# Optimization experiments

Hardware: AMD Instinct MI355X
Metric: run time of the kernel (lower is better)

Reference implementation:

```python
import jax, jax.numpy as jnp
import numpy as np
from jax import lax

DIM = 256
NI, NS, NP = 8, 4, 16
H = W = 36
SCALE = 20.0
POOL = 4
EPS_BN = 1e-5


def setup_inputs() -> dict:
    key = jax.random.key(0)
    ks = jax.random.split(key, 20)
    feat = jax.random.normal(ks[0], (NI, NS, DIM, H, W), jnp.float32)
    # proposals in xywh; scaled by 20 inside PrRoIPool, so keep boxes inside the 36x36 map
    xy = jax.random.uniform(ks[1], (NI, NS, NP, 2), jnp.float32) * 1.2
    wh = 0.1 + jax.random.uniform(ks[2], (NI, NS, NP, 2), jnp.float32) * 0.4
    proposals = jnp.concatenate([xy, wh], axis=-1)

    def kaiming(k, shape, fan_in):
        return jax.random.normal(k, shape, jnp.float32) * np.float32(np.sqrt(2.0 / fan_in))

    d = dict(feat=feat, proposals=proposals)
    for i, name in enumerate(['conv1', 'conv2', 'conv3']):
        d[name + '_w'] = kaiming(ks[3 + i], (DIM, DIM, 3, 3), DIM * 9)
        d[name + '_b'] = jnp.zeros((DIM,), jnp.float32)
        d['bn%d_g' % (i + 1)] = jax.random.uniform(ks[6 + i], (DIM,), jnp.float32)
        d['bn%d_b' % (i + 1)] = jnp.zeros((DIM,), jnp.float32)
    d['fc_w'] = kaiming(ks[9], (DIM, DIM * POOL * POOL), DIM * POOL * POOL)
    d['fc_b'] = jnp.zeros((DIM,), jnp.float32)
    d['fcbn_g'] = jax.random.uniform(ks[10], (DIM,), jnp.float32)
    d['fcbn_b'] = jnp.zeros((DIM,), jnp.float32)
    d['iou_w'] = kaiming(ks[11], (1, DIM), DIM)
    d['iou_b'] = jnp.zeros((1,), jnp.float32)
    return d


def _cbr(x, w, b, g, beta):
    # Conv(3x3, pad 1) + BatchNorm (training-mode batch stats) + ReLU
    x = lax.conv_general_dilated(x, w, (1, 1), ((1, 1), (1, 1)),
                                 dimension_numbers=('NCHW', 'OIHW', 'NCHW'))
    x = x + b[None, :, None, None]
    m = x.mean((0, 2, 3), keepdims=True)
    v = x.var((0, 2, 3), keepdims=True)
    x = (x - m) / jnp.sqrt(v + EPS_BN) * g[None, :, None, None] + beta[None, :, None, None]
    return jax.nn.relu(x)


def _trapcum_last(a):
    # trapezoidal cumulative integral along last axis, value 0 at index 0
    mid = 0.5 * (a[..., :-1] + a[..., 1:])
    return jnp.concatenate([jnp.zeros_like(a[..., :1]), jnp.cumsum(mid, axis=-1)], axis=-1)


def _prroi_pool(feat, rois, pooled=POOL, scale=SCALE):
    # Precise RoI pooling: exact double integral of the bilinear interpolant per bin,
    # computed analytically via trapezoidal cumulative integrals of the feature map.
    N, C, Hh, Ww = feat.shape
    Ux = _trapcum_last(feat)                                            # int_0^x f
    Uy = jnp.swapaxes(_trapcum_last(jnp.swapaxes(feat, -1, -2)), -1, -2)  # int_0^y f
    T = jnp.swapaxes(_trapcum_last(jnp.swapaxes(Ux, -1, -2)), -1, -2)     # int_0^y int_0^x f

    b = rois[:, 0].astype(jnp.int32)
    x1, y1, x2, y2 = (rois[:, 1] * scale, rois[:, 2] * scale,
                      rois[:, 3] * scale, rois[:, 4] * scale)
    bw = (x2 - x1) / pooled
    bh = (y2 - y1) / pooled
    grid = jnp.arange(pooled + 1, dtype=feat.dtype)
    xs = jnp.clip(x1[:, None] + bw[:, None] * grid, 0.0, Ww - 1)        # (R, P+1)
    ys = jnp.clip(y1[:, None] + bh[:, None] * grid, 0.0, Hh - 1)
    wx = jnp.clip(jnp.floor(xs), 0, Ww - 2).astype(jnp.int32)
    hy = jnp.clip(jnp.floor(ys), 0, Hh - 2).astype(jnp.int32)
    sx = xs - wx.astype(feat.dtype)
    sy = ys - hy.astype(feat.dtype)
    px1 = 0.5 * sx * sx
    px0 = sx - px1
    py1 = 0.5 * sy * sy
    py0 = sy - py1

    def g(arr, hi, wi):
        # gather per-RoI values -> (R, P+1, P+1, C), rows index y, cols index x
        return arr[b[:, None, None], :, hi[:, :, None], wi[:, None, :]]

    px0e = px0[:, None, :, None]
    px1e = px1[:, None, :, None]
    py0e = py0[:, :, None, None]
    py1e = py1[:, :, None, None]
    h0, h1 = hy, hy + 1
    w0, w1 = wx, wx + 1
    # antiderivative G(X, Y) = int_0^Y int_0^X f of the bilinear interpolant
    G = (g(T, h0, w0)
         + g(Uy, h0, w0) * px0e + g(Uy, h0, w1) * px1e
         + py0e * (g(Ux, h0, w0) + g(feat, h0, w0) * px0e + g(feat, h0, w1) * px1e)
         + py1e * (g(Ux, h1, w0) + g(feat, h1, w0) * px0e + g(feat, h1, w1) * px1e))
    # per-bin integral via inclusion-exclusion on the (P+1)x(P+1) corner grid
    d = G[:, 1:, 1:] - G[:, :-1, 1:] - G[:, 1:, :-1] + G[:, :-1, :-1]   # (R, P, P, C)
    area = (bw * bh)[:, None, None, None]
    out = jnp.where(area > 1e-8, d / jnp.maximum(area, 1e-8), 0.0)
    return jnp.transpose(out, (0, 3, 1, 2))  # (R, C, P, P)


def reference(feat, proposals, conv1_w, conv1_b, bn1_g, bn1_b, conv2_w, conv2_b,
              bn2_g, bn2_b, conv3_w, conv3_b, bn3_g, bn3_b, fc_w, fc_b,
              fcbn_g, fcbn_b, iou_w, iou_b):
    ni, ns = proposals.shape[0], proposals.shape[1]
    x = feat.reshape(-1, *feat.shape[-3:])
    x = _cbr(x, conv1_w, conv1_b, bn1_g, bn1_b)
    x = _cbr(x, conv2_w, conv2_b, bn2_g, bn2_b)
    x = _cbr(x, conv3_w, conv3_b, bn3_g, bn3_b)

    props = proposals.reshape(ni * ns, -1, 4)
    B, P = props.shape[0], props.shape[1]
    xyxy = jnp.concatenate([props[..., 0:2], props[..., 0:2] + props[..., 2:4]], axis=-1)
    bidx = jnp.broadcast_to(jnp.arange(B, dtype=props.dtype)[:, None, None], (B, P, 1))
    rois = jnp.concatenate([bidx, xyxy], axis=-1).reshape(-1, 5)

    rf = _prroi_pool(x, rois)                       # (B*P, C, 4, 4)
    fcx = rf.reshape(rf.shape[0], -1) @ fc_w.T + fc_b
    m = fcx.mean(0)
    v = fcx.var(0)
    fcx = jax.nn.relu((fcx - m) / jnp.sqrt(v + EPS_BN) * fcbn_g + fcbn_b)
    iou = fcx @ iou_w.T + iou_b                     # (B*P, 1)
    return iou.reshape(ni, ns, -1)
```

## Files before the change

kernel.cpp:

```cpp
#include <hip/hip_runtime.h>
#include <hip/hip_bf16.h>
#include <stdint.h>

#define CDIM 256
#define HH 36
#define WW 36
#define NPX 1296
#define PW 38
#define PPIX 1444
#define NIMG 32
#define NROI 512
#define FCK 4096
#define EPS_BN 1e-5f
#define SBLK 192

typedef __bf16 bf16;
typedef __bf16 bf16x8 __attribute__((ext_vector_type(8)));
typedef float f32x4 __attribute__((ext_vector_type(4)));
typedef unsigned short us8 __attribute__((ext_vector_type(8)));

#define GLD16(g, l) __builtin_amdgcn_global_load_lds( \
    (__attribute__((address_space(1))) void*)(g),     \
    (__attribute__((address_space(3))) void*)(l), 16, 0, 0)

__global__ void k_wconv3(const float* __restrict__ w0, const float* __restrict__ w1,
                         const float* __restrict__ w2, bf16* __restrict__ wb) {
  int l = blockIdx.y;
  const float* ws = (l == 0) ? w0 : (l == 1) ? w1 : w2;
  bf16* dst = wb + (size_t)l * 9 * CDIM * CDIM;
  int i = blockIdx.x * 256 + threadIdx.x;
  if (i >= 9 * CDIM * CDIM) return;
  int tap = i / (CDIM * CDIM);
  int rem = i - tap * (CDIM * CDIM);
  int co = rem >> 8, ci = rem & 255;
  dst[i] = (bf16)ws[(size_t)(co * CDIM + ci) * 9 + tap];
}

__global__ void k_cast(const float* __restrict__ src, bf16* __restrict__ dst, int nElem) {
  int i = blockIdx.x * 256 + threadIdx.x;
  if (i < nElem) dst[i] = (bf16)src[i];
}

__global__ void k_convert(const float* __restrict__ feat, bf16* __restrict__ xp) {
  __shared__ bf16 tile[CDIM * 38];
  int h = blockIdx.x, n = blockIdx.y, t = threadIdx.x;
  const float* src = feat + (size_t)n * CDIM * NPX + (size_t)h * WW;
#pragma unroll 4
  for (int i = 0; i < 36; ++i) {
    int f = i * 256 + t;
    int c = (int)(((unsigned)f * 7282u) >> 18);
    int w = f - c * 36;
    tile[c * 38 + w] = (bf16)src[(size_t)c * NPX + w];
  }
  __syncthreads();
  bf16* dst = xp + (size_t)n * PPIX * CDIM + ((h + 1) * PW + 1) * CDIM + t;
#pragma unroll 4
  for (int w = 0; w < 36; ++w) dst[w * CDIM] = tile[t * 38 + w];
}

__global__ __launch_bounds__(256) void k_conv(
    const bf16* __restrict__ xp, const bf16* __restrict__ wb,
    bf16* __restrict__ y)
{
  __shared__ __align__(16) bf16 ldsA[2][4096];
  __shared__ __align__(16) bf16 ldsB[2][4096];
  const int tid = threadIdx.x;
  const int wave = tid >> 6, lane = tid & 63;
  const int pxt = blockIdx.x, cot = blockIdx.y, n = blockIdx.z;

  const int q = lane >> 2;
  const int gsw = (lane & 3) ^ ((q >> 1) & 3);
  const int rA = wave * 32 + q;
  const bf16* aS0 = wb + (size_t)(cot * 128 + rA) * CDIM + gsw * 8;
  const bf16* aS1 = aS0 + 16 * CDIM;
  int pxa = pxt * 128 + rA;       if (pxa > NPX - 1) pxa = NPX - 1;
  int pxb = pxt * 128 + rA + 16;  if (pxb > NPX - 1) pxb = NPX - 1;
  const int ha = pxa / 36, wa = pxa - ha * 36;
  const int hb = pxb / 36, wbv = pxb - hb * 36;
  const bf16* bS0 = xp + (size_t)n * (PPIX * CDIM) + ((ha + 1) * PW + (wa + 1)) * CDIM + gsw * 8;
  const bf16* bS1 = xp + (size_t)n * (PPIX * CDIM) + ((hb + 1) * PW + (wbv + 1)) * CDIM + gsw * 8;

  const int fr = lane & 15, fg = lane >> 4;
  const int fsw = (fg ^ ((fr >> 1) & 3)) * 8;
  const int wco = wave >> 1, wpx = wave & 1;
  const int aoff = (wco * 64 + fr) * 32 + fsw;
  const int boff = (wpx * 64 + fr) * 32 + fsw;

  f32x4 acc[4][4];
#pragma unroll
  for (int i = 0; i < 4; ++i)
#pragma unroll
    for (int j = 0; j < 4; ++j) acc[i][j] = f32x4{0.f, 0.f, 0.f, 0.f};

  {
    const int xoff = -(PW + 1) * CDIM;
    GLD16(aS0, &ldsA[0][wave * 1024]);
    GLD16(aS1, &ldsA[0][wave * 1024 + 512]);
    GLD16(bS0 + xoff, &ldsB[0][wave * 1024]);
    GLD16(bS1 + xoff, &ldsB[0][wave * 1024 + 512]);
  }

#pragma unroll 2
  for (int k = 0; k < 72; ++k) {
    const int buf = k & 1;
    __syncthreads();
    if (k + 1 < 72) {
      const int kn = k + 1;
      const int tap = kn >> 3, ci0 = (kn & 7) << 5;
      const int dh = tap / 3 - 1, dw = tap - (tap / 3) * 3 - 1;
      const int woff = tap * (CDIM * CDIM) + ci0;
      const int xoff = (dh * PW + dw) * CDIM + ci0;
      const int nb = buf ^ 1;
      GLD16(aS0 + woff, &ldsA[nb][wave * 1024]);
      GLD16(aS1 + woff, &ldsA[nb][wave * 1024 + 512]);
      GLD16(bS0 + xoff, &ldsB[nb][wave * 1024]);
      GLD16(bS1 + xoff, &ldsB[nb][wave * 1024 + 512]);
    }
    bf16x8 av[4], bv[4];
#pragma unroll
    for (int i = 0; i < 4; ++i) av[i] = *(const bf16x8*)&ldsA[buf][aoff + i * 512];
#pragma unroll
    for (int j = 0; j < 4; ++j) bv[j] = *(const bf16x8*)&ldsB[buf][boff + j * 512];
#pragma unroll
    for (int i = 0; i < 4; ++i)
#pragma unroll
      for (int j = 0; j < 4; ++j)
        acc[i][j] = __builtin_amdgcn_mfma_f32_16x16x32_bf16(av[i], bv[j], acc[i][j], 0, 0, 0);
  }

#pragma unroll
  for (int j = 0; j < 4; ++j) {
    const int px = pxt * 128 + wpx * 64 + j * 16 + fr;
    if (px < NPX) {
      bf16* dst = y + ((size_t)n * NPX + px) * CDIM + cot * 128 + wco * 64 + fg * 4;
#pragma unroll
      for (int i = 0; i < 4; ++i) {
        f32x4 a = acc[i][j];
        union { bf16 b4[4]; ushort4 u4; } pk;
        pk.b4[0] = (bf16)a[0]; pk.b4[1] = (bf16)a[1];
        pk.b4[2] = (bf16)a[2]; pk.b4[3] = (bf16)a[3];
        *(ushort4*)(dst + i * 16) = pk.u4;
      }
    }
  }
}

__global__ void k_statsb(const bf16* __restrict__ y, float* __restrict__ psum,
                         float* __restrict__ psq) {
  __shared__ float lsum[8][256];
  __shared__ float lsq[8][256];
  int t = threadIdx.x;
  int c8 = (t & 31) * 8, rg = t >> 5;
  size_t row0 = (size_t)blockIdx.x * 216 + rg;
  float s[8], qq[8];
#pragma unroll
  for (int k = 0; k < 8; ++k) { s[k] = 0.f; qq[k] = 0.f; }
  for (int i = 0; i < 27; ++i) {
    const bf16* p = y + (row0 + (size_t)i * 8) * CDIM + c8;
    union { bf16 b8[8]; us8 u; } v;
    v.u = *(const us8*)p;
#pragma unroll
    for (int k = 0; k < 8; ++k) {
      float f = (float)v.b8[k];
      s[k] += f; qq[k] += f * f;
    }
  }
#pragma unroll
  for (int k = 0; k < 8; ++k) { lsum[rg][c8 + k] = s[k]; lsq[rg][c8 + k] = qq[k]; }
  __syncthreads();
  float ss = 0.f, sq2 = 0.f;
#pragma unroll
  for (int g = 0; g < 8; ++g) { ss += lsum[g][t]; sq2 += lsq[g][t]; }
  psum[blockIdx.x * 256 + t] = ss;
  psq[blockIdx.x * 256 + t] = sq2;
}

__global__ void k_sred(const float* __restrict__ psum, const float* __restrict__ psq,
                       float* __restrict__ su, float* __restrict__ sq) {
  int c = threadIdx.x;
  float s = 0.f, q = 0.f;
  for (int i = 0; i < SBLK; ++i) { s += psum[i * 256 + c]; q += psq[i * 256 + c]; }
  su[c] = s; sq[c] = q;
}

__global__ void k_stats(const float* __restrict__ x, float* __restrict__ sum,
                        float* __restrict__ ssq, int rpb) {
  int c = threadIdx.x;
  size_t base = (size_t)blockIdx.x * rpb;
  float s = 0.f, s2 = 0.f;
  for (int i = 0; i < rpb; ++i) {
    float v = x[(base + i) * CDIM + c];
    s += v; s2 += v * v;
  }
  atomicAdd(&sum[c], s);
  atomicAdd(&ssq[c], s2);
}

__global__ void k_finalize(const float* __restrict__ sum, const float* __restrict__ ssq,
                           const float* __restrict__ g, const float* __restrict__ b,
                           float* __restrict__ sc, float* __restrict__ sh, float invn) {
  int c = threadIdx.x;
  float m = sum[c] * invn;
  float v = ssq[c] * invn - m * m;
  float s = g[c] * rsqrtf(v + EPS_BN);
  sc[c] = s;
  sh[c] = b[c] - m * s;
}

__global__ void k_normalize(const bf16* __restrict__ y, const float* __restrict__ sc,
                            const float* __restrict__ sh, bf16* __restrict__ xp) {
  int t = threadIdx.x;
  int n = blockIdx.y;
  int px = blockIdx.x * 8 + (t >> 5);
  int c8 = (t & 31) * 8;
  const bf16* srcp = y + ((size_t)n * NPX + px) * CDIM + c8;
  union { bf16 b8[8]; us8 u; } in, outp;
  in.u = *(const us8*)srcp;
  int h = px / 36, w = px - h * 36;
#pragma unroll
  for (int i = 0; i < 8; ++i) {
    float v = (float)in.b8[i];
    outp.b8[i] = (bf16)fmaxf(v * sc[c8 + i] + sh[c8 + i], 0.f);
  }
  *(us8*)(xp + (size_t)n * PPIX * CDIM + ((h + 1) * PW + (w + 1)) * CDIM + c8) = outp.u;
}

__global__ void k_p1(const bf16* __restrict__ y, const float* __restrict__ sc,
                     const float* __restrict__ sh, float* __restrict__ Ux) {
  int c = threadIdx.x, h = blockIdx.x, n = blockIdx.y;
  const bf16* row = y + ((size_t)n * NPX + h * WW) * CDIM + c;
  float* orow = Ux + ((size_t)n * NPX + h * WW) * CDIM + c;
  float s = sc[c], t = sh[c];
  float prev = fmaxf((float)row[0] * s + t, 0.f);
  float run = 0.f;
  orow[0] = 0.f;
  for (int w = 1; w < WW; ++w) {
    float cur = fmaxf((float)row[w * CDIM] * s + t, 0.f);
    run += 0.5f * (prev + cur);
    orow[w * CDIM] = run;
    prev = cur;
  }
}

__global__ void k_p2(const bf16* __restrict__ y, const float* __restrict__ sc,
                     const float* __restrict__ sh, const float* __restrict__ Ux,
                     float* __restrict__ Uy, float* __restrict__ T) {
  int c = threadIdx.x, w = blockIdx.x, n = blockIdx.y;
  size_t base = (size_t)n * NPX * CDIM + (size_t)w * CDIM + c;
  float s = sc[c], t = sh[c];
  float prevF = fmaxf((float)y[base] * s + t, 0.f);
  float prevU = Ux[base];
  float runF = 0.f, runU = 0.f;
  Uy[base] = 0.f; T[base] = 0.f;
  for (int h = 1; h < HH; ++h) {
    size_t idx = base + (size_t)h * WW * CDIM;
    float f = fmaxf((float)y[idx] * s + t, 0.f);
    float u = Ux[idx];
    runF += 0.5f * (prevF + f);
    runU += 0.5f * (prevU + u);
    Uy[idx] = runF; T[idx] = runU;
    prevF = f; prevU = u;
  }
}

__global__ __launch_bounds__(128) void k_pool(
    const bf16* __restrict__ y, const float* __restrict__ sc,
    const float* __restrict__ sh, const float* __restrict__ Ux,
    const float* __restrict__ Uy, const float* __restrict__ T,
    const float* __restrict__ props, bf16* __restrict__ rf) {
  int roi = blockIdx.x;
  int c = blockIdx.y * 128 + threadIdx.x;
  int b = roi >> 4;
  const float* pr = props + (size_t)roi * 4;
  float x1 = pr[0] * 20.f, yy1 = pr[1] * 20.f;
  float x2 = (pr[0] + pr[2]) * 20.f, yy2 = (pr[1] + pr[3]) * 20.f;
  float bw = (x2 - x1) * 0.25f, bh = (yy2 - yy1) * 0.25f;
  float px0a[5], px1a[5], py0a[5], py1a[5];
  int wx[5], hy[5];
#pragma unroll
  for (int j = 0; j < 5; ++j) {
    float xs = fminf(fmaxf(x1 + bw * j, 0.f), 35.f);
    int wi = (int)floorf(xs); wi = wi < 0 ? 0 : (wi > 34 ? 34 : wi);
    float sx = xs - (float)wi;
    float p1 = 0.5f * sx * sx;
    wx[j] = wi; px1a[j] = p1; px0a[j] = sx - p1;
    float ys = fminf(fmaxf(yy1 + bh * j, 0.f), 35.f);
    int hi = (int)floorf(ys); hi = hi < 0 ? 0 : (hi > 34 ? 34 : hi);
    float sy = ys - (float)hi;
    float q1 = 0.5f * sy * sy;
    hy[j] = hi; py1a[j] = q1; py0a[j] = sy - q1;
  }
  float s = sc[c], tt = sh[c];
  const float* yb  = (const float*)nullptr;
  const size_t nb = (size_t)b * NPX * CDIM + c;
  const bf16* ybb = y + nb;
  const float* Uxb = Ux + nb;
  const float* Uyb = Uy + nb;
  const float* Tb  = T + nb;
  (void)yb;
  float G[5][5];
#pragma unroll
  for (int i = 0; i < 5; ++i) {
    int h0 = hy[i];
    int rb0 = h0 * (WW * CDIM), rb1 = rb0 + WW * CDIM;
#pragma unroll
    for (int j = 0; j < 5; ++j) {
      int w0 = wx[j];
      int i00 = rb0 + w0 * CDIM;
      int i01 = i00 + CDIM;
      int i10 = rb1 + w0 * CDIM;
      int i11 = i10 + CDIM;
      float f00 = fmaxf((float)ybb[i00] * s + tt, 0.f);
      float f01 = fmaxf((float)ybb[i01] * s + tt, 0.f);
      float f10 = fmaxf((float)ybb[i10] * s + tt, 0.f);
      float f11 = fmaxf((float)ybb[i11] * s + tt, 0.f);
      G[i][j] = Tb[i00] + Uyb[i00] * px0a[j] + Uyb[i01] * px1a[j]
              + py0a[i] * (Uxb[i00] + f00 * px0a[j] + f01 * px1a[j])
              + py1a[i] * (Uxb[i10] + f10 * px0a[j] + f11 * px1a[j]);
    }
  }
  float area = bw * bh;
  float inv = area > 1e-8f ? 1.f / area : 0.f;
  bf16 outv[16];
#pragma unroll
  for (int i = 0; i < 4; ++i)
#pragma unroll
    for (int j = 0; j < 4; ++j) {
      float d = G[i + 1][j + 1] - G[i][j + 1] - G[i + 1][j] + G[i][j];
      outv[i * 4 + j] = (bf16)(d * inv);
    }
  bf16* dst = rf + (size_t)roi * FCK + c * 16;
  *(us8*)(dst)     = *(us8*)&outv[0];
  *(us8*)(dst + 8) = *(us8*)&outv[8];
}

__global__ __launch_bounds__(256) void k_fcgemm(const bf16* __restrict__ rf,
                                                const bf16* __restrict__ fw,
                                                float* __restrict__ fcp) {
  int tid = threadIdx.x, wave = tid >> 6, lane = tid & 63;
  int wo = wave >> 1, wr = wave & 1;
  int rt = blockIdx.x, ot = blockIdx.y, ks = blockIdx.z;
  int fr = lane & 15, fg = lane >> 4;
  const bf16* ap = fw + (size_t)(ot * 64 + wo * 32 + fr) * FCK + ks * 512 + fg * 8;
  const bf16* bp = rf + (size_t)(rt * 64 + wr * 32 + fr) * FCK + ks * 512 + fg * 8;
  f32x4 acc[2][2];
#pragma unroll
  for (int i = 0; i < 2; ++i)
#pragma unroll
    for (int j = 0; j < 2; ++j) acc[i][j] = f32x4{0.f, 0.f, 0.f, 0.f};
#pragma unroll 4
  for (int k = 0; k < 512; k += 32) {
    bf16x8 a0 = *(const bf16x8*)(ap + k);
    bf16x8 a1 = *(const bf16x8*)(ap + 16 * FCK + k);
    bf16x8 b0 = *(const bf16x8*)(bp + k);
    bf16x8 b1 = *(const bf16x8*)(bp + 16 * FCK + k);
    acc[0][0] = __builtin_amdgcn_mfma_f32_16x16x32_bf16(a0, b0, acc[0][0], 0, 0, 0);
    acc[0][1] = __builtin_amdgcn_mfma_f32_16x16x32_bf16(a0, b1, acc[0][1], 0, 0, 0);
    acc[1][0] = __builtin_amdgcn_mfma_f32_16x16x32_bf16(a1, b0, acc[1][0], 0, 0, 0);
    acc[1][1] = __builtin_amdgcn_mfma_f32_16x16x32_bf16(a1, b1, acc[1][1], 0, 0, 0);
  }
#pragma unroll
  for (int i = 0; i < 2; ++i)
#pragma unroll
    for (int j = 0; j < 2; ++j) {
      int o = ot * 64 + wo * 32 + i * 16 + fg * 4;
      int r = rt * 64 + wr * 32 + j * 16 + fr;
      *(f32x4*)(fcp + ((size_t)ks * NROI + r) * CDIM + o) = acc[i][j];
    }
}

__global__ void k_fcred(const float* __restrict__ fcp, float* __restrict__ fcx) {
  int r = blockIdx.x, o = threadIdx.x;
  float s = 0.f;
#pragma unroll
  for (int ks = 0; ks < 8; ++ks) s += fcp[((size_t)ks * NROI + r) * CDIM + o];
  fcx[(size_t)r * CDIM + o] = s;
}

__global__ void k_iou(const float* __restrict__ fcx, const float* __restrict__ sc,
                      const float* __restrict__ sh, const float* __restrict__ iw,
                      const float* __restrict__ ib, float* __restrict__ out) {
  __shared__ float red[4];
  int roi = blockIdx.x, t = threadIdx.x;
  float v = fcx[(size_t)roi * CDIM + t];
  v = fmaxf(v * sc[t] + sh[t], 0.f) * iw[t];
#pragma unroll
  for (int o = 32; o > 0; o >>= 1) v += __shfl_down(v, o);
  if ((t & 63) == 0) red[t >> 6] = v;
  __syncthreads();
  if (t == 0) out[roi] = red[0] + red[1] + red[2] + red[3] + ib[0];
}

extern "C" void kernel_launch(void* const* d_in, const int* in_sizes, int n_in,
                              void* d_out, int out_size, void* d_ws, size_t ws_size,
                              hipStream_t stream) {
  (void)in_sizes; (void)n_in; (void)out_size;
  const float* feat  = (const float*)d_in[0];
  const float* props = (const float*)d_in[1];
  const float* convw[3] = {(const float*)d_in[2], (const float*)d_in[6], (const float*)d_in[10]};
  const float* bng[3]   = {(const float*)d_in[4], (const float*)d_in[8], (const float*)d_in[12]};
  const float* bnb[3]   = {(const float*)d_in[5], (const float*)d_in[9], (const float*)d_in[13]};
  const float* fcw  = (const float*)d_in[14];
  const float* fcg  = (const float*)d_in[16];
  const float* fcbb = (const float*)d_in[17];
  const float* iw   = (const float*)d_in[18];
  const float* ib   = (const float*)d_in[19];
  float* out = (float*)d_out;

  char* w = (char*)d_ws;
  size_t off = 0;
  auto take = [&](size_t sz) -> char* { char* p = w + off; off += (sz + 255) & ~(size_t)255; return p; };
  const size_t SZ_XP = (size_t)NIMG * PPIX * CDIM * 2;
  const size_t SZ_YB = (size_t)NIMG * NPX * CDIM * 2;
  const size_t SZ_U  = (size_t)NIMG * NPX * CDIM * 4;
  const size_t SZ_P  = (size_t)SBLK * 256 * 4;
  bf16*  xp0 = (bf16*)take(SZ_XP);
  bf16*  xp1 = (bf16*)take(SZ_XP);
  bf16*  y   = (bf16*)take(SZ_YB);
  float* Ux  = (float*)take(SZ_U);
  float* Uy  = (float*)take(SZ_U);
  float* Tt  = (float*)take(SZ_U);
  bf16*  wball = (bf16*)take((size_t)3 * 9 * CDIM * CDIM * 2);
  bf16*  fwb = (bf16*)take((size_t)CDIM * FCK * 2);
  bf16*  rfb = (bf16*)take((size_t)NROI * FCK * 2);
  float* fcx = (float*)take((size_t)NROI * CDIM * 4);
  float* psum = (float*)take(SZ_P);
  float* psq  = (float*)take(SZ_P);
  float* stat = (float*)take(8 * 256 * 4);
  float* scsh = (float*)take(8 * 256 * 4);
  if (off > ws_size) return;

  float* fcp = Ux;

  hipMemsetAsync(xp0, 0, SZ_XP * 2, stream);
  hipMemsetAsync(stat, 0, 8 * 256 * 4, stream);

  k_wconv3<<<dim3(2304, 3), 256, 0, stream>>>(convw[0], convw[1], convw[2], wball);
  k_cast<<<dim3(4096), 256, 0, stream>>>(fcw, fwb, CDIM * FCK);
  k_convert<<<dim3(HH, NIMG), 256, 0, stream>>>(feat, xp0);

  for (int l = 0; l < 3; ++l) {
    bf16* xin = (l == 1) ? xp1 : xp0;
    bf16* wbl = wball + (size_t)l * 9 * CDIM * CDIM;
    k_conv<<<dim3(11, 2, NIMG), 256, 0, stream>>>(xin, wbl, y);
    float* su = stat + l * 512; float* sq = su + 256;
    k_statsb<<<dim3(SBLK), 256, 0, stream>>>(y, psum, psq);
    k_sred<<<dim3(1), 256, 0, stream>>>(psum, psq, su, sq);
    float* sc = scsh + l * 512; float* sh = sc + 256;
    k_finalize<<<dim3(1), 256, 0, stream>>>(su, sq, bng[l], bnb[l], sc, sh, 1.f / 41472.f);
    if (l < 2) {
      bf16* xo = (l == 0) ? xp1 : xp0;
      k_normalize<<<dim3(NPX / 8, NIMG), 256, 0, stream>>>(y, sc, sh, xo);
    }
  }
  float* sc3 = scsh + 2 * 512; float* sh3 = sc3 + 256;
  k_p1<<<dim3(HH, NIMG), 256, 0, stream>>>(y, sc3, sh3, Ux);
  k_p2<<<dim3(WW, NIMG), 256, 0, stream>>>(y, sc3, sh3, Ux, Uy, Tt);
  k_pool<<<dim3(NROI, 2), 128, 0, stream>>>(y, sc3, sh3, Ux, Uy, Tt, props, rfb);
  k_fcgemm<<<dim3(8, 4, 8), 256, 0, stream>>>(rfb, fwb, fcp);
  k_fcred<<<dim3(NROI), 256, 0, stream>>>(fcp, fcx);
  float* fsu = stat + 3 * 512; float* fsq = fsu + 256;
  k_stats<<<dim3(8), 256, 0, stream>>>(fcx, fsu, fsq, 64);
  float* fsc = scsh + 3 * 512; float* fsh = fsc + 256;
  k_finalize<<<dim3(1), 256, 0, stream>>>(fsu, fsq, fcg, fcbb, fsc, fsh, 1.f / 512.f);
  k_iou<<<dim3(NROI), 256, 0, stream>>>(fcx, fsc, fsh, iw, ib, out);
}
```

Measured before the change: 528.3 us.

## Compute PrRoI bins directly with hat-integral weights, dropping prefix-integral kernels

Replaces the two-pass trapezoidal prefix-integral tables (Ux, Uy, T) and their two sequential scan kernels with direct per-bin integration. Each bin weights nearby pixels using separable weights taken from the antiderivative of the bilinear hat function. This removes about 3 fp32 full-size feature-map writes and reads plus two poorly parallel scan launches. In exchange, k_pool now reads up to 5x5 bf16 pixels per bin, with clamped indexing and skipping of zero weights, which is more per-ROI work and more scattered gathers.

Result: faster. 490.2 us (-7.2%).

```diff
diff --git a/kernel.cpp b/kernel.cpp
--- a/kernel.cpp
+++ b/kernel.cpp
@@ -225,49 +225,16 @@
   *(us8*)(xp + (size_t)n * PPIX * CDIM + ((h + 1) * PW + (w + 1)) * CDIM + c8) = outp.u;
 }
 
-__global__ void k_p1(const bf16* __restrict__ y, const float* __restrict__ sc,
-                     const float* __restrict__ sh, float* __restrict__ Ux) {
-  int c = threadIdx.x, h = blockIdx.x, n = blockIdx.y;
-  const bf16* row = y + ((size_t)n * NPX + h * WW) * CDIM + c;
-  float* orow = Ux + ((size_t)n * NPX + h * WW) * CDIM + c;
-  float s = sc[c], t = sh[c];
-  float prev = fmaxf((float)row[0] * s + t, 0.f);
-  float run = 0.f;
-  orow[0] = 0.f;
-  for (int w = 1; w < WW; ++w) {
-    float cur = fmaxf((float)row[w * CDIM] * s + t, 0.f);
-    run += 0.5f * (prev + cur);
-    orow[w * CDIM] = run;
-    prev = cur;
-  }
-}
-
-__global__ void k_p2(const bf16* __restrict__ y, const float* __restrict__ sc,
-                     const float* __restrict__ sh, const float* __restrict__ Ux,
-                     float* __restrict__ Uy, float* __restrict__ T) {
-  int c = threadIdx.x, w = blockIdx.x, n = blockIdx.y;
-  size_t base = (size_t)n * NPX * CDIM + (size_t)w * CDIM + c;
-  float s = sc[c], t = sh[c];
-  float prevF = fmaxf((float)y[base] * s + t, 0.f);
-  float prevU = Ux[base];
-  float runF = 0.f, runU = 0.f;
-  Uy[base] = 0.f; T[base] = 0.f;
-  for (int h = 1; h < HH; ++h) {
-    size_t idx = base + (size_t)h * WW * CDIM;
-    float f = fmaxf((float)y[idx] * s + t, 0.f);
-    float u = Ux[idx];
-    runF += 0.5f * (prevF + f);
-    runU += 0.5f * (prevU + u);
-    Uy[idx] = runF; T[idx] = runU;
-    prevF = f; prevU = u;
-  }
+__device__ __forceinline__ float hatH(float u) {
+  u = fminf(fmaxf(u, -1.f), 1.f);
+  float p = u + 1.f;
+  return (u < 0.f) ? 0.5f * p * p : 0.5f + u * (1.f - 0.5f * u);
 }
 
 __global__ __launch_bounds__(128) void k_pool(
     const bf16* __restrict__ y, const float* __restrict__ sc,
-    const float* __restrict__ sh, const float* __restrict__ Ux,
-    const float* __restrict__ Uy, const float* __restrict__ T,
-    const float* __restrict__ props, bf16* __restrict__ rf) {
+    const float* __restrict__ sh, const float* __restrict__ props,
+    bf16* __restrict__ rf) {
   int roi = blockIdx.x;
   int c = blockIdx.y * 128 + threadIdx.x;
   int b = roi >> 4;
@@ -275,60 +242,73 @@
   float x1 = pr[0] * 20.f, yy1 = pr[1] * 20.f;
   float x2 = (pr[0] + pr[2]) * 20.f, yy2 = (pr[1] + pr[3]) * 20.f;
   float bw = (x2 - x1) * 0.25f, bh = (yy2 - yy1) * 0.25f;
-  float px0a[5], px1a[5], py0a[5], py1a[5];
-  int wx[5], hy[5];
+
+  float xs[5], ys[5];
 #pragma unroll
   for (int j = 0; j < 5; ++j) {
-    float xs = fminf(fmaxf(x1 + bw * j, 0.f), 35.f);
-    int wi = (int)floorf(xs); wi = wi < 0 ? 0 : (wi > 34 ? 34 : wi);
-    float sx = xs - (float)wi;
-    float p1 = 0.5f * sx * sx;
-    wx[j] = wi; px1a[j] = p1; px0a[j] = sx - p1;
-    float ys = fminf(fmaxf(yy1 + bh * j, 0.f), 35.f);
-    int hi = (int)floorf(ys); hi = hi < 0 ? 0 : (hi > 34 ? 34 : hi);
-    float sy = ys - (float)hi;
-    float q1 = 0.5f * sy * sy;
-    hy[j] = hi; py1a[j] = q1; py0a[j] = sy - q1;
-  }
-  float s = sc[c], tt = sh[c];
-  const float* yb  = (const float*)nullptr;
-  const size_t nb = (size_t)b * NPX * CDIM + c;
-  const bf16* ybb = y + nb;
-  const float* Uxb = Ux + nb;
-  const float* Uyb = Uy + nb;
-  const float* Tb  = T + nb;
-  (void)yb;
-  float G[5][5];
-#pragma unroll
-  for (int i = 0; i < 5; ++i) {
-    int h0 = hy[i];
-    int rb0 = h0 * (WW * CDIM), rb1 = rb0 + WW * CDIM;
-#pragma unroll
-    for (int j = 0; j < 5; ++j) {
-      int w0 = wx[j];
-      int i00 = rb0 + w0 * CDIM;
-      int i01 = i00 + CDIM;
-      int i10 = rb1 + w0 * CDIM;
-      int i11 = i10 + CDIM;
-      float f00 = fmaxf((float)ybb[i00] * s + tt, 0.f);
-      float f01 = fmaxf((float)ybb[i01] * s + tt, 0.f);
-      float f10 = fmaxf((float)ybb[i10] * s + tt, 0.f);
-      float f11 = fmaxf((float)ybb[i11] * s + tt, 0.f);
-      G[i][j] = Tb[i00] + Uyb[i00] * px0a[j] + Uyb[i01] * px1a[j]
-              + py0a[i] * (Uxb[i00] + f00 * px0a[j] + f01 * px1a[j])
-              + py1a[i] * (Uxb[i10] + f10 * px0a[j] + f11 * px1a[j]);
-    }
-  }
+    xs[j] = fminf(fmaxf(x1 + bw * j, 0.f), 35.f);
+    ys[j] = fminf(fmaxf(yy1 + bh * j, 0.f), 35.f);
+  }
+  float wxv[4][5], wyv[4][5];
+  int sx[4], sy[4];
+#pragma unroll
+  for (int j = 0; j < 4; ++j) {
+    float a = xs[j], bb = xs[j + 1];
+    int s = (int)floorf(a);
+    sx[j] = s;
+#pragma unroll
+    for (int k = 0; k < 5; ++k) {
+      float w = (float)(s + k);
+      wxv[j][k] = hatH(bb - w) - hatH(a - w);
+    }
+    float ay = ys[j], by = ys[j + 1];
+    int t = (int)floorf(ay);
+    sy[j] = t;
+#pragma unroll
+    for (int k = 0; k < 5; ++k) {
+      float w = (float)(t + k);
+      wyv[j][k] = hatH(by - w) - hatH(ay - w);
+    }
+  }
+
+  float s_ = sc[c], t_ = sh[c];
+  const bf16* yb = y + (size_t)b * NPX * CDIM + c;
+  float acc[4][4];
+#pragma unroll
+  for (int i = 0; i < 4; ++i)
+#pragma unroll
+    for (int j = 0; j < 4; ++j) acc[i][j] = 0.f;
+
+#pragma unroll
+  for (int i = 0; i < 4; ++i) {
+#pragma unroll
+    for (int ky = 0; ky < 5; ++ky) {
+      float wy = wyv[i][ky];
+      if (wy == 0.f) continue;
+      int h = sy[i] + ky; if (h > 35) h = 35;
+      const bf16* rowp = yb + h * (WW * CDIM);
+#pragma unroll
+      for (int j = 0; j < 4; ++j) {
+        float rd = 0.f;
+#pragma unroll
+        for (int kx = 0; kx < 5; ++kx) {
+          int w = sx[j] + kx; if (w > 35) w = 35;
+          float f = fmaxf((float)rowp[w * CDIM] * s_ + t_, 0.f);
+          rd += wxv[j][kx] * f;
+        }
+        acc[i][j] += wy * rd;
+      }
+    }
+  }
+
   float area = bw * bh;
   float inv = area > 1e-8f ? 1.f / area : 0.f;
   bf16 outv[16];
 #pragma unroll
   for (int i = 0; i < 4; ++i)
 #pragma unroll
-    for (int j = 0; j < 4; ++j) {
-      float d = G[i + 1][j + 1] - G[i][j + 1] - G[i + 1][j] + G[i][j];
-      outv[i * 4 + j] = (bf16)(d * inv);
-    }
+    for (int j = 0; j < 4; ++j)
+      outv[i * 4 + j] = (bf16)(acc[i][j] * inv);
   bf16* dst = rf + (size_t)roi * FCK + c * 16;
   *(us8*)(dst)     = *(us8*)&outv[0];
   *(us8*)(dst + 8) = *(us8*)&outv[8];
@@ -412,25 +392,20 @@
   auto take = [&](size_t sz) -> char* { char* p = w + off; off += (sz + 255) & ~(size_t)255; return p; };
   const size_t SZ_XP = (size_t)NIMG * PPIX * CDIM * 2;
   const size_t SZ_YB = (size_t)NIMG * NPX * CDIM * 2;
-  const size_t SZ_U  = (size_t)NIMG * NPX * CDIM * 4;
   const size_t SZ_P  = (size_t)SBLK * 256 * 4;
   bf16*  xp0 = (bf16*)take(SZ_XP);
   bf16*  xp1 = (bf16*)take(SZ_XP);
   bf16*  y   = (bf16*)take(SZ_YB);
-  float* Ux  = (float*)take(SZ_U);
-  float* Uy  = (float*)take(SZ_U);
-  float* Tt  = (float*)take(SZ_U);
   bf16*  wball = (bf16*)take((size_t)3 * 9 * CDIM * CDIM * 2);
   bf16*  fwb = (bf16*)take((size_t)CDIM * FCK * 2);
   bf16*  rfb = (bf16*)take((size_t)NROI * FCK * 2);
   float* fcx = (float*)take((size_t)NROI * CDIM * 4);
+  float* fcp = (float*)take((size_t)8 * NROI * CDIM * 4);
   float* psum = (float*)take(SZ_P);
   float* psq  = (float*)take(SZ_P);
   float* stat = (float*)take(8 * 256 * 4);
   float* scsh = (float*)take(8 * 256 * 4);
   if (off > ws_size) return;
-
-  float* fcp = Ux;
 
   hipMemsetAsync(xp0, 0, SZ_XP * 2, stream);
   hipMemsetAsync(stat, 0, 8 * 256 * 4, stream);
@@ -454,9 +429,7 @@
     }
   }
   float* sc3 = scsh + 2 * 512; float* sh3 = sc3 + 256;
-  k_p1<<<dim3(HH, NIMG), 256, 0, stream>>>(y, sc3, sh3, Ux);
-  k_p2<<<dim3(WW, NIMG), 256, 0, stream>>>(y, sc3, sh3, Ux, Uy, Tt);
-  k_pool<<<dim3(NROI, 2), 128, 0, stream>>>(y, sc3, sh3, Ux, Uy, Tt, props, rfb);
+  k_pool<<<dim3(NROI, 2), 128, 0, stream>>>(y, sc3, sh3, props, rfb);
   k_fcgemm<<<dim3(8, 4, 8), 256, 0, stream>>>(rfb, fwb, fcp);
   k_fcred<<<dim3(NROI), 256, 0, stream>>>(fcp, fcx);
   float* fsu = stat + 3 * 512; float* fsq = fsu + 256;
```
